# Kernel tuning notes

Measured on AMD Instinct MI355X. Metric: run time of the kernel, lower is better.

## Reference

```python
import jax, jax.numpy as jnp
import numpy as np

FAR_DELTA = 1e10
TRANS_EPS = 1e-10


def setup_inputs() -> dict:
    key = jax.random.key(0)
    k1, k2, k3, k4 = jax.random.split(key, 4)
    N, S = 262144, 48  # rays (512x512 image), samples per ray
    ray_samples = jax.random.uniform(k1, (N, S, 3), dtype=jnp.float32)
    densities = jax.random.uniform(k2, (N, S, 1), dtype=jnp.float32)
    rgb = jax.random.uniform(k3, (N, S, 3), dtype=jnp.float32)
    background_color = jax.random.uniform(k4, (N, 3), dtype=jnp.float32)
    return {
        "ray_samples": ray_samples,
        "densities": densities,
        "rgb": rgb,
        "background_color": background_color,
    }


def render_weights(ray_samples, densities):
    # delta_i = ||x_{i+1} - x_i||, last delta set to 1e10 (ray goes to infinity)
    diff = ray_samples[..., 1:, :] - ray_samples[..., :-1, :]
    delta = jnp.linalg.norm(diff, axis=-1, keepdims=True)          # [N, S-1, 1]
    delta = jnp.concatenate(
        [delta, jnp.full_like(delta[..., -1:, :], FAR_DELTA)], axis=-2
    )                                                               # [N, S, 1]
    alpha = 1.0 - jnp.exp(-jax.nn.relu(densities) * delta)          # [N, S, 1]
    # transmittance T_i = prod_{j<i} (1 - alpha_j + eps)
    trans = jnp.cumprod(
        jnp.concatenate(
            [jnp.ones_like(alpha[..., :1, :]), 1.0 - alpha + TRANS_EPS], axis=-2
        ),
        axis=-2,
    )[..., :-1, :]                                                  # [N, S, 1]
    weights = alpha * trans                                         # [N, S, 1]
    return weights


def reference(ray_samples, densities, rgb, background_color):
    weights = render_weights(ray_samples, densities)
    rendered_rgb = jnp.sum(weights * rgb, axis=-2)                  # [N, 3]
    accumulated_alpha = jnp.sum(weights, axis=-2)                   # [N, 1]
    rendered_rgb = rendered_rgb + background_color * (1.0 - accumulated_alpha)
    accumulation = accumulated_alpha.squeeze(-1)                    # [N]
    return rendered_rgb, accumulation, weights
```

## Files before the change

### kernel.cpp

```cpp
#include <hip/hip_runtime.h>
#include <math.h>

#define FAR_DELTA 1e10f
#define TRANS_EPS 1e-10f

template<int CTRL>
__device__ __forceinline__ float dppf(float x, float old) {
    return __int_as_float(__builtin_amdgcn_update_dpp(
        __float_as_int(old), __float_as_int(x), CTRL, 0xF, 0xF, false));
}

__global__ __launch_bounds__(256) void nerf_render_kernel(
    const float* __restrict__ xyz,
    const float* __restrict__ dens,
    const float* __restrict__ rgb,
    const float* __restrict__ bg,
    float* __restrict__ out_rgb,
    float* __restrict__ out_acc,
    float* __restrict__ out_w,
    int N)
{
    const int tid = blockIdx.x * 256 + threadIdx.x;
    const int li  = threadIdx.x & 15;
    const int ray = tid >> 4;
    if (ray >= N) return;

    const size_t base = (size_t)ray * 48 + (size_t)li * 3;

    const float* px = xyz + base * 3;
    float x0 = px[0], y0 = px[1], z0 = px[2];
    float x1 = px[3], y1 = px[4], z1 = px[5];
    float x2 = px[6], y2 = px[7], z2 = px[8];

    const float* pd = dens + base;
    float d0 = pd[0], d1 = pd[1], d2 = pd[2];

    const float* pc = rgb + base * 3;
    float r0 = pc[0], g0 = pc[1], b0 = pc[2];
    float r1 = pc[3], g1 = pc[4], b1 = pc[5];
    float r2 = pc[6], g2 = pc[7], b2 = pc[8];

    float xn = dppf<0x101>(x0, 0.f);
    float yn = dppf<0x101>(y0, 0.f);
    float zn = dppf<0x101>(z0, 0.f);

    float dx, dy, dz;
    dx = x1 - x0; dy = y1 - y0; dz = z1 - z0;
    float delta0 = sqrtf(dx * dx + dy * dy + dz * dz);
    dx = x2 - x1; dy = y2 - y1; dz = z2 - z1;
    float delta1 = sqrtf(dx * dx + dy * dy + dz * dz);
    float delta2;
    if (li == 15) {
        delta2 = FAR_DELTA;
    } else {
        dx = xn - x2; dy = yn - y2; dz = zn - z2;
        delta2 = sqrtf(dx * dx + dy * dy + dz * dz);
    }

    float e0 = __expf(-fmaxf(d0, 0.f) * delta0);
    float e1 = __expf(-fmaxf(d1, 0.f) * delta1);
    float e2 = __expf(-fmaxf(d2, 0.f) * delta2);
    float a0 = 1.f - e0, a1 = 1.f - e1, a2 = 1.f - e2;
    float q0 = e0 + TRANS_EPS, q1 = e1 + TRANS_EPS, q2 = e2 + TRANS_EPS;

    float m = q0 * q1 * q2;
    float t = dppf<0x111>(m, 1.f);
    t *= dppf<0x111>(t, 1.f);
    t *= dppf<0x112>(t, 1.f);
    t *= dppf<0x114>(t, 1.f);
    t *= dppf<0x118>(t, 1.f);

    float T0 = t, T1 = t * q0, T2 = T1 * q1;
    float w0 = a0 * T0, w1 = a1 * T1, w2 = a2 * T2;

    float* pw = out_w + base;
    pw[0] = w0; pw[1] = w1; pw[2] = w2;

    float sr = w0 * r0 + w1 * r1 + w2 * r2;
    float sg = w0 * g0 + w1 * g1 + w2 * g2;
    float sb = w0 * b0 + w1 * b1 + w2 * b2;
    float sw = w0 + w1 + w2;

    sr += dppf<0xB1>(sr, 0.f); sg += dppf<0xB1>(sg, 0.f);
    sb += dppf<0xB1>(sb, 0.f); sw += dppf<0xB1>(sw, 0.f);
    sr += dppf<0x4E>(sr, 0.f); sg += dppf<0x4E>(sg, 0.f);
    sb += dppf<0x4E>(sb, 0.f); sw += dppf<0x4E>(sw, 0.f);
    sr += dppf<0x141>(sr, 0.f); sg += dppf<0x141>(sg, 0.f);
    sb += dppf<0x141>(sb, 0.f); sw += dppf<0x141>(sw, 0.f);
    sr += dppf<0x140>(sr, 0.f); sg += dppf<0x140>(sg, 0.f);
    sb += dppf<0x140>(sb, 0.f); sw += dppf<0x140>(sw, 0.f);

    if (li == 0) {
        const float* pb = bg + (size_t)ray * 3;
        float inv = 1.f - sw;
        float* po = out_rgb + (size_t)ray * 3;
        po[0] = sr + pb[0] * inv;
        po[1] = sg + pb[1] * inv;
        po[2] = sb + pb[2] * inv;
        out_acc[ray] = sw;
    }
}

extern "C" void kernel_launch(void* const* d_in, const int* in_sizes, int n_in,
                              void* d_out, int out_size, void* d_ws, size_t ws_size,
                              hipStream_t stream) {
    const float* xyz  = (const float*)d_in[0];
    const float* dens = (const float*)d_in[1];
    const float* rgb  = (const float*)d_in[2];
    const float* bg   = (const float*)d_in[3];

    const int N = in_sizes[3] / 3;

    float* out     = (float*)d_out;
    float* out_rgb = out;
    float* out_acc = out + (size_t)N * 3;
    float* out_w   = out + (size_t)N * 4;

    const int grid = (N + 15) / 16;
    nerf_render_kernel<<<grid, 256, 0, stream>>>(xyz, dens, rgb, bg,
                                                 out_rgb, out_acc, out_w, N);
}
```

Before: 78.48 us.

## Stage ray data through shared memory with coalesced float4 loads and stores

Each block of 16 rays now copies its xyz, rgb, density and background data into LDS using fully coalesced float4 global loads, computes from LDS, then writes weights and per-ray outputs back with float4 stores. Before this, each lane read strided 36-byte chunks directly from global memory, which coalesces poorly. The cost is about 20KB of LDS per block, two barriers, and extra LDS traffic with bank conflicts from the stride-9 access, all of which may reduce occupancy.

```diff
diff --git a/kernel.cpp b/kernel.cpp
--- a/kernel.cpp
+++ b/kernel.cpp
@@ -3,6 +3,8 @@
 
 #define FAR_DELTA 1e10f
 #define TRANS_EPS 1e-10f
+#define RPB 16
+#define S  48
 
 template<int CTRL>
 __device__ __forceinline__ float dppf(float x, float old) {
@@ -20,84 +22,131 @@
     float* __restrict__ out_w,
     int N)
 {
-    const int tid = blockIdx.x * 256 + threadIdx.x;
-    const int li  = threadIdx.x & 15;
-    const int ray = tid >> 4;
-    if (ray >= N) return;
+    __shared__ float s_xyz[RPB * S * 3];
+    __shared__ float s_rgb[RPB * S * 3];
+    __shared__ float s_den[RPB * S];
+    __shared__ float s_bg [RPB * 3];
+    __shared__ float s_or [RPB * 3];
+    __shared__ float s_oa [RPB];
 
-    const size_t base = (size_t)ray * 48 + (size_t)li * 3;
+    const int t    = threadIdx.x;
+    const int ray0 = blockIdx.x * RPB;
+    const int nray = min(RPB, N - ray0);
 
-    const float* px = xyz + base * 3;
-    float x0 = px[0], y0 = px[1], z0 = px[2];
-    float x1 = px[3], y1 = px[4], z1 = px[5];
-    float x2 = px[6], y2 = px[7], z2 = px[8];
+    if (nray == RPB) {
+        const float4* gx = (const float4*)(xyz  + (size_t)ray0 * (S * 3));
+        const float4* gc = (const float4*)(rgb  + (size_t)ray0 * (S * 3));
+        const float4* gd = (const float4*)(dens + (size_t)ray0 * S);
+        const float4* gb = (const float4*)(bg   + (size_t)ray0 * 3);
+        float4* sx = (float4*)s_xyz;
+        float4* sc = (float4*)s_rgb;
+        float4* sd = (float4*)s_den;
+        float4* sb = (float4*)s_bg;
+        sx[t]       = gx[t];
+        sx[t + 256] = gx[t + 256];
+        sc[t]       = gc[t];
+        sc[t + 256] = gc[t + 256];
+        if (t < 64)  { sx[t + 512] = gx[t + 512]; sc[t + 512] = gc[t + 512]; }
+        if (t < 192) sd[t] = gd[t];
+        if (t < 12)  sb[t] = gb[t];
+    } else {
+        const int nf3 = nray * S * 3, nf1 = nray * S, nfb = nray * 3;
+        for (int i = t; i < nf3; i += 256) s_xyz[i] = xyz[(size_t)ray0 * (S*3) + i];
+        for (int i = t; i < nf3; i += 256) s_rgb[i] = rgb[(size_t)ray0 * (S*3) + i];
+        for (int i = t; i < nf1; i += 256) s_den[i] = dens[(size_t)ray0 * S + i];
+        for (int i = t; i < nfb; i += 256) s_bg[i]  = bg[(size_t)ray0 * 3 + i];
+    }
+    __syncthreads();
 
-    const float* pd = dens + base;
-    float d0 = pd[0], d1 = pd[1], d2 = pd[2];
+    const int g  = t >> 4;
+    const int li = t & 15;
 
-    const float* pc = rgb + base * 3;
-    float r0 = pc[0], g0 = pc[1], b0 = pc[2];
-    float r1 = pc[3], g1 = pc[4], b1 = pc[5];
-    float r2 = pc[6], g2 = pc[7], b2 = pc[8];
+    if (g < nray) {
+        const float* px = s_xyz + g * (S * 3) + li * 9;
+        float x0 = px[0], y0 = px[1], z0 = px[2];
+        float x1 = px[3], y1 = px[4], z1 = px[5];
+        float x2 = px[6], y2 = px[7], z2 = px[8];
 
-    float xn = dppf<0x101>(x0, 0.f);
-    float yn = dppf<0x101>(y0, 0.f);
-    float zn = dppf<0x101>(z0, 0.f);
+        const float* pd = s_den + g * S + li * 3;
+        float d0 = pd[0], d1 = pd[1], d2 = pd[2];
 
-    float dx, dy, dz;
-    dx = x1 - x0; dy = y1 - y0; dz = z1 - z0;
-    float delta0 = sqrtf(dx * dx + dy * dy + dz * dz);
-    dx = x2 - x1; dy = y2 - y1; dz = z2 - z1;
-    float delta1 = sqrtf(dx * dx + dy * dy + dz * dz);
-    float delta2;
-    if (li == 15) {
-        delta2 = FAR_DELTA;
+        const float* pc = s_rgb + g * (S * 3) + li * 9;
+        float r0 = pc[0], g0 = pc[1], b0 = pc[2];
+        float r1 = pc[3], g1 = pc[4], b1 = pc[5];
+        float r2 = pc[6], g2 = pc[7], b2 = pc[8];
+
+        float xn = dppf<0x101>(x0, 0.f);
+        float yn = dppf<0x101>(y0, 0.f);
+        float zn = dppf<0x101>(z0, 0.f);
+
+        float dx, dy, dz;
+        dx = x1 - x0; dy = y1 - y0; dz = z1 - z0;
+        float delta0 = sqrtf(dx * dx + dy * dy + dz * dz);
+        dx = x2 - x1; dy = y2 - y1; dz = z2 - z1;
+        float delta1 = sqrtf(dx * dx + dy * dy + dz * dz);
+        float delta2;
+        if (li == 15) {
+            delta2 = FAR_DELTA;
+        } else {
+            dx = xn - x2; dy = yn - y2; dz = zn - z2;
+            delta2 = sqrtf(dx * dx + dy * dy + dz * dz);
+        }
+
+        float e0 = __expf(-fmaxf(d0, 0.f) * delta0);
+        float e1 = __expf(-fmaxf(d1, 0.f) * delta1);
+        float e2 = __expf(-fmaxf(d2, 0.f) * delta2);
+        float a0 = 1.f - e0, a1 = 1.f - e1, a2 = 1.f - e2;
+        float q0 = e0 + TRANS_EPS, q1 = e1 + TRANS_EPS, q2 = e2 + TRANS_EPS;
+
+        float m = q0 * q1 * q2;
+        float tr = dppf<0x111>(m, 1.f);
+        tr *= dppf<0x111>(tr, 1.f);
+        tr *= dppf<0x112>(tr, 1.f);
+        tr *= dppf<0x114>(tr, 1.f);
+        tr *= dppf<0x118>(tr, 1.f);
+
+        float T0 = tr, T1 = tr * q0, T2 = T1 * q1;
+        float w0 = a0 * T0, w1 = a1 * T1, w2 = a2 * T2;
+
+        float* pw = s_den + g * S + li * 3;
+        pw[0] = w0; pw[1] = w1; pw[2] = w2;
+
+        float sr = w0 * r0 + w1 * r1 + w2 * r2;
+        float sg = w0 * g0 + w1 * g1 + w2 * g2;
+        float sb = w0 * b0 + w1 * b1 + w2 * b2;
+        float sw = w0 + w1 + w2;
+
+        sr += dppf<0xB1>(sr, 0.f);  sg += dppf<0xB1>(sg, 0.f);
+        sb += dppf<0xB1>(sb, 0.f);  sw += dppf<0xB1>(sw, 0.f);
+        sr += dppf<0x4E>(sr, 0.f);  sg += dppf<0x4E>(sg, 0.f);
+        sb += dppf<0x4E>(sb, 0.f);  sw += dppf<0x4E>(sw, 0.f);
+        sr += dppf<0x141>(sr, 0.f); sg += dppf<0x141>(sg, 0.f);
+        sb += dppf<0x141>(sb, 0.f); sw += dppf<0x141>(sw, 0.f);
+        sr += dppf<0x140>(sr, 0.f); sg += dppf<0x140>(sg, 0.f);
+        sb += dppf<0x140>(sb, 0.f); sw += dppf<0x140>(sw, 0.f);
+
+        if (li == 0) {
+            float inv = 1.f - sw;
+            s_or[g * 3 + 0] = sr + s_bg[g * 3 + 0] * inv;
+            s_or[g * 3 + 1] = sg + s_bg[g * 3 + 1] * inv;
+            s_or[g * 3 + 2] = sb + s_bg[g * 3 + 2] * inv;
+            s_oa[g] = sw;
+        }
+    }
+    __syncthreads();
+
+    if (nray == RPB) {
+        float4* gw = (float4*)(out_w + (size_t)ray0 * S);
+        if (t < 192) gw[t] = ((const float4*)s_den)[t];
+        float4* gr = (float4*)(out_rgb + (size_t)ray0 * 3);
+        if (t < 12) gr[t] = ((const float4*)s_or)[t];
+        float4* ga = (float4*)(out_acc + ray0);
+        if (t < 4) ga[t] = ((const float4*)s_oa)[t];
     } else {
-        dx = xn - x2; dy = yn - y2; dz = zn - z2;
-        delta2 = sqrtf(dx * dx + dy * dy + dz * dz);
-    }
-
-    float e0 = __expf(-fmaxf(d0, 0.f) * delta0);
-    float e1 = __expf(-fmaxf(d1, 0.f) * delta1);
-    float e2 = __expf(-fmaxf(d2, 0.f) * delta2);
-    float a0 = 1.f - e0, a1 = 1.f - e1, a2 = 1.f - e2;
-    float q0 = e0 + TRANS_EPS, q1 = e1 + TRANS_EPS, q2 = e2 + TRANS_EPS;
-
-    float m = q0 * q1 * q2;
-    float t = dppf<0x111>(m, 1.f);
-    t *= dppf<0x111>(t, 1.f);
-    t *= dppf<0x112>(t, 1.f);
-    t *= dppf<0x114>(t, 1.f);
-    t *= dppf<0x118>(t, 1.f);
-
-    float T0 = t, T1 = t * q0, T2 = T1 * q1;
-    float w0 = a0 * T0, w1 = a1 * T1, w2 = a2 * T2;
-
-    float* pw = out_w + base;
-    pw[0] = w0; pw[1] = w1; pw[2] = w2;
-
-    float sr = w0 * r0 + w1 * r1 + w2 * r2;
-    float sg = w0 * g0 + w1 * g1 + w2 * g2;
-    float sb = w0 * b0 + w1 * b1 + w2 * b2;
-    float sw = w0 + w1 + w2;
-
-    sr += dppf<0xB1>(sr, 0.f); sg += dppf<0xB1>(sg, 0.f);
-    sb += dppf<0xB1>(sb, 0.f); sw += dppf<0xB1>(sw, 0.f);
-    sr += dppf<0x4E>(sr, 0.f); sg += dppf<0x4E>(sg, 0.f);
-    sb += dppf<0x4E>(sb, 0.f); sw += dppf<0x4E>(sw, 0.f);
-    sr += dppf<0x141>(sr, 0.f); sg += dppf<0x141>(sg, 0.f);
-    sb += dppf<0x141>(sb, 0.f); sw += dppf<0x141>(sw, 0.f);
-    sr += dppf<0x140>(sr, 0.f); sg += dppf<0x140>(sg, 0.f);
-    sb += dppf<0x140>(sb, 0.f); sw += dppf<0x140>(sw, 0.f);
-
-    if (li == 0) {
-        const float* pb = bg + (size_t)ray * 3;
-        float inv = 1.f - sw;
-        float* po = out_rgb + (size_t)ray * 3;
-        po[0] = sr + pb[0] * inv;
-        po[1] = sg + pb[1] * inv;
-        po[2] = sb + pb[2] * inv;
-        out_acc[ray] = sw;
+        const int nw = nray * S, no = nray * 3;
+        for (int i = t; i < nw; i += 256) out_w[(size_t)ray0 * S + i] = s_den[i];
+        for (int i = t; i < no; i += 256) out_rgb[(size_t)ray0 * 3 + i] = s_or[i];
+        for (int i = t; i < nray; i += 256) out_acc[ray0 + i] = s_oa[i];
     }
 }
 
@@ -116,7 +165,7 @@
     float* out_acc = out + (size_t)N * 3;
     float* out_w   = out + (size_t)N * 4;
 
-    const int grid = (N + 15) / 16;
+    const int grid = (N + RPB - 1) / RPB;
     nerf_render_kernel<<<grid, 256, 0, stream>>>(xyz, dens, rgb, bg,
                                                  out_rgb, out_acc, out_w, N);
 }
```

After: 81.79 us. 4.2% more time.

## Use persistent grid-stride blocks with double-buffered ray loads and nontemporal stores

Applied to the files above, without the earlier changes.

Replaces the one-tile-per-block launch with a persistent grid capped at 2048 blocks that loops over tiles. It software-pipelines the loop with two register sets, issuing the next tile's loads before computing the current one, so memory latency overlaps with compute. Output stores become nontemporal to keep write traffic out of the cache. The extra register set may lower occupancy, and a capped grid can leave bandwidth unused on a purely memory-bound kernel.

```diff
diff --git a/kernel.cpp b/kernel.cpp
--- a/kernel.cpp
+++ b/kernel.cpp
@@ -3,6 +3,7 @@
 
 #define FAR_DELTA 1e10f
 #define TRANS_EPS 1e-10f
+#define S 48
 
 template<int CTRL>
 __device__ __forceinline__ float dppf(float x, float old) {
@@ -10,56 +11,53 @@
         __float_as_int(old), __float_as_int(x), CTRL, 0xF, 0xF, false));
 }
 
-__global__ __launch_bounds__(256) void nerf_render_kernel(
-    const float* __restrict__ xyz,
-    const float* __restrict__ dens,
-    const float* __restrict__ rgb,
-    const float* __restrict__ bg,
-    float* __restrict__ out_rgb,
-    float* __restrict__ out_acc,
-    float* __restrict__ out_w,
-    int N)
+struct Regs {
+    float x0,y0,z0,x1,y1,z1,x2,y2,z2;
+    float d0,d1,d2;
+    float r0,g0,b0,r1,g1,b1,r2,g2,b2;
+};
+
+__device__ __forceinline__ void load_ray(Regs& R,
+        const float* __restrict__ xyz, const float* __restrict__ dens,
+        const float* __restrict__ rgb, long long ray, int li)
 {
-    const int tid = blockIdx.x * 256 + threadIdx.x;
-    const int li  = threadIdx.x & 15;
-    const int ray = tid >> 4;
-    if (ray >= N) return;
+    const size_t base = (size_t)ray * S + (size_t)li * 3;
+    const float* px = xyz + base * 3;
+    R.x0 = px[0]; R.y0 = px[1]; R.z0 = px[2];
+    R.x1 = px[3]; R.y1 = px[4]; R.z1 = px[5];
+    R.x2 = px[6]; R.y2 = px[7]; R.z2 = px[8];
+    const float* pd = dens + base;
+    R.d0 = pd[0]; R.d1 = pd[1]; R.d2 = pd[2];
+    const float* pc = rgb + base * 3;
+    R.r0 = pc[0]; R.g0 = pc[1]; R.b0 = pc[2];
+    R.r1 = pc[3]; R.g1 = pc[4]; R.b1 = pc[5];
+    R.r2 = pc[6]; R.g2 = pc[7]; R.b2 = pc[8];
+}
 
-    const size_t base = (size_t)ray * 48 + (size_t)li * 3;
+__device__ __forceinline__ void compute_ray(const Regs& R,
+        const float* __restrict__ bg, float* __restrict__ out_rgb,
+        float* __restrict__ out_acc, float* __restrict__ out_w,
+        long long ray, int li)
+{
+    float xn = dppf<0x101>(R.x0, 0.f);
+    float yn = dppf<0x101>(R.y0, 0.f);
+    float zn = dppf<0x101>(R.z0, 0.f);
 
-    const float* px = xyz + base * 3;
-    float x0 = px[0], y0 = px[1], z0 = px[2];
-    float x1 = px[3], y1 = px[4], z1 = px[5];
-    float x2 = px[6], y2 = px[7], z2 = px[8];
-
-    const float* pd = dens + base;
-    float d0 = pd[0], d1 = pd[1], d2 = pd[2];
-
-    const float* pc = rgb + base * 3;
-    float r0 = pc[0], g0 = pc[1], b0 = pc[2];
-    float r1 = pc[3], g1 = pc[4], b1 = pc[5];
-    float r2 = pc[6], g2 = pc[7], b2 = pc[8];
-
-    float xn = dppf<0x101>(x0, 0.f);
-    float yn = dppf<0x101>(y0, 0.f);
-    float zn = dppf<0x101>(z0, 0.f);
-
-    float dx, dy, dz;
-    dx = x1 - x0; dy = y1 - y0; dz = z1 - z0;
+    float dx = R.x1 - R.x0, dy = R.y1 - R.y0, dz = R.z1 - R.z0;
     float delta0 = sqrtf(dx * dx + dy * dy + dz * dz);
-    dx = x2 - x1; dy = y2 - y1; dz = z2 - z1;
+    dx = R.x2 - R.x1; dy = R.y2 - R.y1; dz = R.z2 - R.z1;
     float delta1 = sqrtf(dx * dx + dy * dy + dz * dz);
     float delta2;
     if (li == 15) {
         delta2 = FAR_DELTA;
     } else {
-        dx = xn - x2; dy = yn - y2; dz = zn - z2;
+        dx = xn - R.x2; dy = yn - R.y2; dz = zn - R.z2;
         delta2 = sqrtf(dx * dx + dy * dy + dz * dz);
     }
 
-    float e0 = __expf(-fmaxf(d0, 0.f) * delta0);
-    float e1 = __expf(-fmaxf(d1, 0.f) * delta1);
-    float e2 = __expf(-fmaxf(d2, 0.f) * delta2);
+    float e0 = __expf(-fmaxf(R.d0, 0.f) * delta0);
+    float e1 = __expf(-fmaxf(R.d1, 0.f) * delta1);
+    float e2 = __expf(-fmaxf(R.d2, 0.f) * delta2);
     float a0 = 1.f - e0, a1 = 1.f - e1, a2 = 1.f - e2;
     float q0 = e0 + TRANS_EPS, q1 = e1 + TRANS_EPS, q2 = e2 + TRANS_EPS;
 
@@ -73,18 +71,20 @@
     float T0 = t, T1 = t * q0, T2 = T1 * q1;
     float w0 = a0 * T0, w1 = a1 * T1, w2 = a2 * T2;
 
-    float* pw = out_w + base;
-    pw[0] = w0; pw[1] = w1; pw[2] = w2;
+    float* pw = out_w + (size_t)ray * S + (size_t)li * 3;
+    __builtin_nontemporal_store(w0, pw + 0);
+    __builtin_nontemporal_store(w1, pw + 1);
+    __builtin_nontemporal_store(w2, pw + 2);
 
-    float sr = w0 * r0 + w1 * r1 + w2 * r2;
-    float sg = w0 * g0 + w1 * g1 + w2 * g2;
-    float sb = w0 * b0 + w1 * b1 + w2 * b2;
+    float sr = w0 * R.r0 + w1 * R.r1 + w2 * R.r2;
+    float sg = w0 * R.g0 + w1 * R.g1 + w2 * R.g2;
+    float sb = w0 * R.b0 + w1 * R.b1 + w2 * R.b2;
     float sw = w0 + w1 + w2;
 
-    sr += dppf<0xB1>(sr, 0.f); sg += dppf<0xB1>(sg, 0.f);
-    sb += dppf<0xB1>(sb, 0.f); sw += dppf<0xB1>(sw, 0.f);
-    sr += dppf<0x4E>(sr, 0.f); sg += dppf<0x4E>(sg, 0.f);
-    sb += dppf<0x4E>(sb, 0.f); sw += dppf<0x4E>(sw, 0.f);
+    sr += dppf<0xB1>(sr, 0.f);  sg += dppf<0xB1>(sg, 0.f);
+    sb += dppf<0xB1>(sb, 0.f);  sw += dppf<0xB1>(sw, 0.f);
+    sr += dppf<0x4E>(sr, 0.f);  sg += dppf<0x4E>(sg, 0.f);
+    sb += dppf<0x4E>(sb, 0.f);  sw += dppf<0x4E>(sw, 0.f);
     sr += dppf<0x141>(sr, 0.f); sg += dppf<0x141>(sg, 0.f);
     sb += dppf<0x141>(sb, 0.f); sw += dppf<0x141>(sw, 0.f);
     sr += dppf<0x140>(sr, 0.f); sg += dppf<0x140>(sg, 0.f);
@@ -94,10 +94,50 @@
         const float* pb = bg + (size_t)ray * 3;
         float inv = 1.f - sw;
         float* po = out_rgb + (size_t)ray * 3;
-        po[0] = sr + pb[0] * inv;
-        po[1] = sg + pb[1] * inv;
-        po[2] = sb + pb[2] * inv;
-        out_acc[ray] = sw;
+        __builtin_nontemporal_store(sr + pb[0] * inv, po + 0);
+        __builtin_nontemporal_store(sg + pb[1] * inv, po + 1);
+        __builtin_nontemporal_store(sb + pb[2] * inv, po + 2);
+        __builtin_nontemporal_store(sw, out_acc + ray);
+    }
+}
+
+__global__ __launch_bounds__(256) void nerf_render_kernel(
+    const float* __restrict__ xyz,
+    const float* __restrict__ dens,
+    const float* __restrict__ rgb,
+    const float* __restrict__ bg,
+    float* __restrict__ out_rgb,
+    float* __restrict__ out_acc,
+    float* __restrict__ out_w,
+    int N, int ntiles)
+{
+    const int li    = threadIdx.x & 15;
+    const int group = threadIdx.x >> 4;
+    const int stride = gridDim.x;
+
+    long long tCur = blockIdx.x;
+    if (tCur >= ntiles) return;
+
+    Regs A, B;
+    long long rayA = tCur * 16 + group;
+    if (rayA < N) load_ray(A, xyz, dens, rgb, rayA, li);
+
+    for (;;) {
+        long long tNext = tCur + stride;
+        bool hn = tNext < ntiles;
+        long long rayB = tNext * 16 + group;
+        if (hn && rayB < N) load_ray(B, xyz, dens, rgb, rayB, li);
+        if (rayA < N) compute_ray(A, bg, out_rgb, out_acc, out_w, rayA, li);
+        if (!hn) break;
+        tCur = tNext;
+
+        tNext = tCur + stride;
+        hn = tNext < ntiles;
+        rayA = tNext * 16 + group;
+        if (hn && rayA < N) load_ray(A, xyz, dens, rgb, rayA, li);
+        if (rayB < N) compute_ray(B, bg, out_rgb, out_acc, out_w, rayB, li);
+        if (!hn) break;
+        tCur = tNext;
     }
 }
 
@@ -116,7 +156,9 @@
     float* out_acc = out + (size_t)N * 3;
     float* out_w   = out + (size_t)N * 4;
 
-    const int grid = (N + 15) / 16;
+    const int ntiles = (N + 15) / 16;
+    const int grid = ntiles < 2048 ? ntiles : 2048;
     nerf_render_kernel<<<grid, 256, 0, stream>>>(xyz, dens, rgb, bg,
-                                                 out_rgb, out_acc, out_w, N);
+                                                 out_rgb, out_acc, out_w,
+                                                 N, ntiles);
 }
```

After: 85.34 us. +8.7%, slower.
